# Kernel tuning notes

Hardware: AMD Instinct MI355X
Metric: run time of the kernel (lower is better)

## Reference

```python
import jax, jax.numpy as jnp
import numpy as np

EMB = 1024
HEADS = 16
HEAD_DIM = EMB // HEADS
FF = 4 * EMB
B, S = 4, 2048


def gelu_tanh(x):
    c = jnp.sqrt(jnp.asarray(2.0 / jnp.pi, x.dtype))
    return 0.5 * x * (1.0 + jnp.tanh(c * (x + 0.044715 * x ** 3)))


def layernorm(x, g, b, eps=1e-5):
    mu = jnp.mean(x, axis=-1, keepdims=True)
    var = jnp.var(x, axis=-1, keepdims=True)
    return (x - mu) * jax.lax.rsqrt(var + eps) * g + b


def setup_inputs() -> dict:
    key = jax.random.key(0)
    ks = jax.random.split(key, 12)
    s = 0.02
    return {
        "x": jax.random.normal(ks[0], (B, S, EMB), jnp.float32),
        "Wq": jax.random.normal(ks[1], (EMB, EMB), jnp.float32) * s,
        "bq": jnp.zeros((EMB,), jnp.float32),
        "Wk": jax.random.normal(ks[2], (EMB, EMB), jnp.float32) * s,
        "bk": jnp.zeros((EMB,), jnp.float32),
        "Wv": jax.random.normal(ks[3], (EMB, EMB), jnp.float32) * s,
        "bv": jnp.zeros((EMB,), jnp.float32),
        "Wo": jax.random.normal(ks[4], (EMB, EMB), jnp.float32) * s,
        "bo": jnp.zeros((EMB,), jnp.float32),
        "W1": jax.random.normal(ks[5], (EMB, FF), jnp.float32) * s,
        "b1": jnp.zeros((FF,), jnp.float32),
        "W2": jax.random.normal(ks[6], (FF, EMB), jnp.float32) * s,
        "b2": jnp.zeros((EMB,), jnp.float32),
        "g1": jnp.ones((EMB,), jnp.float32),
        "be1": jnp.zeros((EMB,), jnp.float32),
        "g2": jnp.ones((EMB,), jnp.float32),
        "be2": jnp.zeros((EMB,), jnp.float32),
    }


def reference(x, Wq, bq, Wk, bk, Wv, bv, Wo, bo, W1, b1, W2, b2, g1, be1, g2, be2):
    b, s, _ = x.shape
    shortcut = x
    h = layernorm(x, g1, be1)
    # QKV projections -> [b, heads, s, head_dim]
    def proj(W, bias):
        return (h @ W + bias).reshape(b, s, HEADS, HEAD_DIM).transpose(0, 2, 1, 3)
    q, k, v = proj(Wq, bq), proj(Wk, bk), proj(Wv, bv)
    scores = jnp.einsum('bhqd,bhkd->bhqk', q, k) / jnp.sqrt(jnp.asarray(HEAD_DIM, x.dtype))
    causal = jnp.triu(jnp.ones((s, s), bool), k=1)  # True above diagonal -> masked
    scores = jnp.where(causal, -jnp.inf, scores)
    probs = jax.nn.softmax(scores, axis=-1)  # dropout p=0 -> identity
    ctx = jnp.einsum('bhqk,bhkd->bhqd', probs, v).transpose(0, 2, 1, 3).reshape(b, s, EMB)
    attn_out = ctx @ Wo + bo
    x = attn_out + shortcut
    shortcut = x
    h = layernorm(x, g2, be2)
    ff = gelu_tanh(h @ W1 + b1) @ W2 + b2
    return ff + shortcut
```

## Files before the change

kernel.cpp:

```cpp
#include <hip/hip_runtime.h>
#include <hip/hip_bf16.h>

#define EMB 1024
#define HEADS 16
#define HDIM 64
#define FFDIM 4096
#define BSZ 4
#define SEQ 2048
#define MROWS (BSZ * SEQ)
#define QKVW 3072
#define VSTRIDE 2080

typedef __attribute__((ext_vector_type(8))) short bf16x8;
typedef __attribute__((ext_vector_type(4))) float f32x4;
typedef __attribute__((ext_vector_type(16))) float f32x16;
typedef __attribute__((ext_vector_type(4))) unsigned short u16x4;
typedef unsigned short u16;

__device__ __forceinline__ float bf2f(u16 u) {
  union { unsigned int i; float f; } c; c.i = ((unsigned int)u) << 16; return c.f;
}
__device__ __forceinline__ u16 f2bf(float f) {
  union { float f; unsigned int i; } c; c.f = f;
  unsigned int i = c.i + 0x7fff + ((c.i >> 16) & 1);
  return (u16)(i >> 16);
}
__device__ __forceinline__ unsigned fbits(float f) {
  union { float f; unsigned u; } c; c.f = f; return c.u;
}
__device__ __forceinline__ unsigned pk2(float e0, float e1) {
  return (fbits(e0) >> 16) | (fbits(e1) & 0xffff0000u);
}
__device__ __forceinline__ f32x16 zero16() {
  f32x16 z;
#pragma unroll
  for (int i = 0; i < 16; ++i) z[i] = 0.f;
  return z;
}
__device__ __forceinline__ void gload16(const u16* g, void* lds) {
  __builtin_amdgcn_global_load_lds(
      (const __attribute__((address_space(1))) void*)g,
      (__attribute__((address_space(3))) void*)lds, 16, 0, 0);
}

__global__ __launch_bounds__(256) void ln_kernel(
    const float* __restrict__ x, const float* __restrict__ g,
    const float* __restrict__ be, u16* __restrict__ out) {
  int w = threadIdx.x >> 6, l = threadIdx.x & 63;
  size_t row = (size_t)blockIdx.x * 4 + w;
  const float* xr = x + row * EMB;
  float f[4][4];
  float s = 0.f, s2 = 0.f;
#pragma unroll
  for (int c = 0; c < 4; ++c) {
    f32x4 v = *(const f32x4*)(xr + c * 256 + l * 4);
#pragma unroll
    for (int j = 0; j < 4; ++j) {
      f[c][j] = v[j];
      s += v[j];
      s2 += v[j] * v[j];
    }
  }
#pragma unroll
  for (int m = 1; m < 64; m <<= 1) {
    s  += __shfl_xor(s, m);
    s2 += __shfl_xor(s2, m);
  }
  float mu = s * (1.f / EMB);
  float var = s2 * (1.f / EMB) - mu * mu;
  float rs = rsqrtf(var + 1e-5f);
#pragma unroll
  for (int c = 0; c < 4; ++c) {
    u16x4 o;
#pragma unroll
    for (int j = 0; j < 4; ++j) {
      int col = c * 256 + l * 4 + j;
      o[j] = f2bf((f[c][j] - mu) * rs * g[col] + be[col]);
    }
    *(u16x4*)(out + row * EMB + c * 256 + l * 4) = o;
  }
}

__global__ __launch_bounds__(256) void transpose_cvt(
    const float* __restrict__ in, u16* __restrict__ out, int R, int C) {
  __shared__ u16 tile[32][33];
  int c0 = blockIdx.x * 32, r0 = blockIdx.y * 32;
  int tx = threadIdx.x, ty = threadIdx.y;
#pragma unroll
  for (int i = ty; i < 32; i += 8)
    tile[i][tx] = f2bf(in[(size_t)(r0 + i) * C + c0 + tx]);
  __syncthreads();
#pragma unroll
  for (int i = ty; i < 32; i += 8)
    out[(size_t)(c0 + i) * R + r0 + tx] = tile[tx][i];
}

__global__ __launch_bounds__(256) void concat_bias(
    const float* __restrict__ a, const float* __restrict__ b,
    const float* __restrict__ c, float* __restrict__ o) {
  int i = blockIdx.x * 256 + threadIdx.x;
  o[i] = i < 1024 ? a[i] : (i < 2048 ? b[i - 1024] : c[i - 2048]);
}

__global__ __launch_bounds__(256) void transpose_v(
    const u16* __restrict__ QKV, u16* __restrict__ Vt) {
  __shared__ u16 tile[32][33];
  int s0 = blockIdx.x * 32, d0 = blockIdx.y * 32, bh = blockIdx.z;
  int h = bh % HEADS, b = bh / HEADS;
  int tx = threadIdx.x, ty = threadIdx.y;
  const u16* src = QKV + (size_t)b * SEQ * QKVW + 2048 + h * HDIM;
  u16* dst = Vt + (size_t)bh * HDIM * VSTRIDE;
#pragma unroll
  for (int i = ty; i < 32; i += 8)
    tile[i][tx] = src[(size_t)(s0 + i) * QKVW + d0 + tx];
  __syncthreads();
#pragma unroll
  for (int i = ty; i < 32; i += 8)
    dst[(size_t)(d0 + i) * VSTRIDE + s0 + tx] = tile[tx][i];
}

__device__ __forceinline__ float gelu_f(float v) {
  float u = 1.5957691216057308f * (v + 0.044715f * v * v * v);
  return v / (1.f + __expf(-u));
}

template <int EPI, typename OT>
__global__ __launch_bounds__(256, 3) void gemm32(
    const u16* __restrict__ A, const u16* __restrict__ Bt,
    const float* __restrict__ bias, const float* __restrict__ res,
    OT* __restrict__ C, int N, int K) {
  __shared__ char lds[32768];
  char* ldsA = lds;
  char* ldsB = lds + 16384;
  int nbn = N >> 7;
  int cpx = gridDim.x >> 3;
  int bid = blockIdx.x;
  int logical = (bid & 7) * cpx + (bid >> 3);
  int mb = logical / nbn, nb = logical % nbn;
  int m0 = mb << 7, n0 = nb << 7;
  int t = threadIdx.x, w = t >> 6, l = t & 63;
  int wr = w >> 1, wc = w & 1;
  int l31 = l & 31, lh = l >> 5;
  int srow8 = l >> 3, sp8 = l & 7;

  f32x16 acc[2][2] = {{zero16(), zero16()}, {zero16(), zero16()}};

  for (int k0 = 0; k0 < K; k0 += 64) {
    __syncthreads();
#pragma unroll
    for (int ps = 0; ps < 4; ++ps) {
      int r = ps * 32 + (w << 3) + srow8;
      int sc = (sp8 ^ (r & 7)) << 3;
      gload16(A + (size_t)(m0 + r) * K + k0 + sc, ldsA + ps * 4096 + (w << 10));
      gload16(Bt + (size_t)(n0 + r) * K + k0 + sc, ldsB + ps * 4096 + (w << 10));
    }
    __syncthreads();
#pragma unroll
    for (int hf = 0; hf < 2; ++hf) {
      bf16x8 afr[2][2], bfr[2][2];
#pragma unroll
      for (int blk = 0; blk < 2; ++blk)
#pragma unroll
        for (int kk = 0; kk < 2; ++kk) {
          int kki = hf * 2 + kk;
          int ra = (wr << 6) + (blk << 5) + l31;
          int rb = (wc << 6) + (blk << 5) + l31;
          int pa = (((kki << 1) + lh) ^ (ra & 7)) << 4;
          int pb = (((kki << 1) + lh) ^ (rb & 7)) << 4;
          afr[blk][kk] = *(const bf16x8*)(ldsA + ra * 128 + pa);
          bfr[blk][kk] = *(const bf16x8*)(ldsB + rb * 128 + pb);
        }
#pragma unroll
      for (int m = 0; m < 2; ++m)
#pragma unroll
        for (int n = 0; n < 2; ++n)
#pragma unroll
          for (int kk = 0; kk < 2; ++kk)
            acc[m][n] = __builtin_amdgcn_mfma_f32_32x32x16_bf16(
                afr[m][kk], bfr[n][kk], acc[m][n], 0, 0, 0);
    }
  }

#pragma unroll
  for (int m = 0; m < 2; ++m)
#pragma unroll
    for (int n = 0; n < 2; ++n) {
      int col = n0 + (wc << 6) + (n << 5) + l31;
      float bcol = bias[col];
      int rbase = m0 + (wr << 6) + (m << 5) + (lh << 2);
#pragma unroll
      for (int reg = 0; reg < 16; ++reg) {
        int row = rbase + (reg & 3) + ((reg >> 2) << 3);
        float v = acc[m][n][reg] + bcol;
        if (EPI & 2) v = gelu_f(v);
        if (EPI & 1) v += res[(size_t)row * N + col];
        if (sizeof(OT) == 2)
          C[(size_t)row * N + col] = (OT)f2bf(v);
        else
          C[(size_t)row * N + col] = (OT)v;
      }
    }
}

#define QKT(ACCS, QF)                                                       \
  do {                                                                      \
    ACCS = zero16();                                                        \
    __builtin_amdgcn_s_setprio(1);                                          \
    _Pragma("unroll") for (int s_ = 0; s_ < 4; ++s_)                        \
        ACCS = __builtin_amdgcn_mfma_f32_32x32x16_bf16(kf[s_], QF[s_],      \
                                                       ACCS, 0, 0, 0);      \
    __builtin_amdgcn_s_setprio(0);                                          \
  } while (0)

#define STEP(ACCS, L, O0, O1, DIAG)                                         \
  do {                                                                      \
    float e_[16];                                                           \
    _Pragma("unroll") for (int i = 0; i < 16; ++i) {                        \
      float sv = ACCS[i];                                                   \
      if (DIAG) {                                                           \
        int kvl = (i & 3) + 8 * (i >> 2) + 4 * g;                           \
        if (kvl > lq) sv = -1e30f;                                          \
      }                                                                     \
      e_[i] = __expf(sv);                                                   \
    }                                                                       \
    float ts = 0.f;                                                         \
    _Pragma("unroll") for (int i = 0; i < 16; ++i) ts += e_[i];             \
    ts += __shfl_xor(ts, 32);                                               \
    L += ts;                                                                \
    _Pragma("unroll") for (int s_ = 0; s_ < 2; ++s_) {                      \
      unsigned plo0 = pk2(e_[8 * s_ + 0], e_[8 * s_ + 1]);                  \
      unsigned plo1 = pk2(e_[8 * s_ + 2], e_[8 * s_ + 3]);                  \
      unsigned phi0 = pk2(e_[8 * s_ + 4], e_[8 * s_ + 5]);                  \
      unsigned phi1 = pk2(e_[8 * s_ + 6], e_[8 * s_ + 7]);                  \
      unsigned recv0 = __shfl_xor(g ? plo0 : phi0, 32);                     \
      unsigned recv1 = __shfl_xor(g ? plo1 : phi1, 32);                     \
      union { unsigned u[4]; bf16x8 v; } pf_;                               \
      pf_.u[0] = g ? recv0 : plo0;                                          \
      pf_.u[1] = g ? recv1 : plo1;                                          \
      pf_.u[2] = g ? phi0 : recv0;                                          \
      pf_.u[3] = g ? phi1 : recv1;                                          \
      __builtin_amdgcn_s_setprio(1);                                        \
      O0 = __builtin_amdgcn_mfma_f32_32x32x16_bf16(vf0[s_], pf_.v, O0,      \
                                                   0, 0, 0);                \
      O1 = __builtin_amdgcn_mfma_f32_32x32x16_bf16(vf1[s_], pf_.v, O1,      \
                                                   0, 0, 0);                \
      __builtin_amdgcn_s_setprio(0);                                        \
    }                                                                       \
  } while (0)

#define STAGE(KV0, BUF)                                                     \
  do {                                                                      \
    char* sb_ = myslab + (BUF) * 8192;                                      \
    _Pragma("unroll") for (int i_ = 0; i_ < 4; ++i_) {                      \
      int r_ = i_ * 8 + (l >> 3);                                           \
      gload16(Kp + (size_t)((KV0) + r_) * QKVW + (((l & 7) ^ (r_ & 7)) << 3),\
              sb_ + i_ * 1024);                                             \
    }                                                                       \
    _Pragma("unroll") for (int i_ = 0; i_ < 4; ++i_) {                      \
      int r_ = i_ * 16 + (l >> 2);                                          \
      gload16(Vt + (size_t)r_ * VSTRIDE + (KV0) + (((l & 3) ^ (r_ & 3)) << 3),\
              sb_ + 4096 + i_ * 1024);                                      \
    }                                                                       \
  } while (0)

#define RDFRAGS(BUF)                                                        \
  do {                                                                      \
    const char* sb_ = myslab + (BUF) * 8192;                                \
    _Pragma("unroll") for (int s_ = 0; s_ < 4; ++s_) {                      \
      int c_ = s_ * 2 + g;                                                  \
      kf[s_] = *(const bf16x8*)(sb_ + lq * 128 + ((c_ ^ (lq & 7)) << 4));   \
    }                                                                       \
    _Pragma("unroll") for (int s_ = 0; s_ < 2; ++s_) {                      \
      int c_ = s_ * 2 + g;                                                  \
      vf0[s_] = *(const bf16x8*)(sb_ + 4096 + lq * 64 +                     \
                                 ((c_ ^ (lq & 3)) << 4));                   \
      vf1[s_] = *(const bf16x8*)(sb_ + 4096 + (32 + lq) * 64 +              \
                                 ((c_ ^ (lq & 3)) << 4));                   \
    }                                                                       \
  } while (0)

#define WRITE_OUT(O0, O1, L, WQ0)                                           \
  do {                                                                      \
    float inv = 1.f / L;                                                    \
    u16* orow = Op + (size_t)((WQ0) + lq) * EMB;                            \
    _Pragma("unroll") for (int dblk = 0; dblk < 2; ++dblk) {                \
      _Pragma("unroll") for (int p = 0; p < 8; ++p) {                       \
        int i0 = 2 * p;                                                     \
        int d = dblk * 32 + 2 * (p & 1) + 8 * (p >> 1) + 4 * g;             \
        float v0 = (dblk ? O1[i0] : O0[i0]) * inv;                          \
        float v1 = (dblk ? O1[i0 + 1] : O0[i0 + 1]) * inv;                  \
        unsigned wd = (unsigned)f2bf(v0) | ((unsigned)f2bf(v1) << 16);      \
        *(unsigned*)(orow + d) = wd;                                        \
      }                                                                     \
    }                                                                       \
  } while (0)

__global__ __launch_bounds__(256, 2) void attn_kernel(
    const u16* __restrict__ QKV, const u16* __restrict__ VtG,
    u16* __restrict__ O) {
  __shared__ char slabs[4][16384];
  int t = threadIdx.x, w = t >> 6, l = t & 63;
  int lq = l & 31, g = l >> 5;
  char* myslab = slabs[w];
  int wid = blockIdx.x * 4 + w;
  int qi = wid & 31, bh = wid >> 5;
  int h = bh & (HEADS - 1), b = bh >> 4;
  int wq0a = qi * 32, wq0b = (63 - qi) * 32;
  int ntA = qi + 1, ntB = 64 - qi;
  const u16* Qp = QKV + (size_t)b * SEQ * QKVW + h * HDIM;
  const u16* Kp = QKV + (size_t)b * SEQ * QKVW + 1024 + h * HDIM;
  const u16* Vt = VtG + (size_t)bh * HDIM * VSTRIDE;
  u16* Op = O + (size_t)b * SEQ * EMB + h * HDIM;

  bf16x8 qfA[4], qfB[4];
#pragma unroll
  for (int s = 0; s < 4; ++s) {
    bf16x8 ra = *(const bf16x8*)(Qp + (size_t)(wq0a + lq) * QKVW + s * 16 + g * 8);
    bf16x8 rb = *(const bf16x8*)(Qp + (size_t)(wq0b + lq) * QKVW + s * 16 + g * 8);
#pragma unroll
    for (int j = 0; j < 8; ++j) {
      qfA[s][j] = (short)f2bf(bf2f((u16)ra[j]) * 0.125f);
      qfB[s][j] = (short)f2bf(bf2f((u16)rb[j]) * 0.125f);
    }
  }

  f32x16 oA0 = zero16(), oA1 = zero16(), oB0 = zero16(), oB1 = zero16();
  f32x16 sA, sB;
  float lA = 0.f, lB = 0.f;
  bf16x8 kf[4], vf0[2], vf1[2];

  STAGE(0, 0);
  for (int ti = 0; ti < ntA; ++ti) {
    STAGE((ti + 1) * 32, (ti + 1) & 1);
    asm volatile("s_waitcnt vmcnt(8)" ::: "memory");
    RDFRAGS(ti & 1);
    QKT(sA, qfA);
    QKT(sB, qfB);
    bool diagA = (ti == ntA - 1);
    STEP(sA, lA, oA0, oA1, diagA);
    STEP(sB, lB, oB0, oB1, false);
  }
  WRITE_OUT(oA0, oA1, lA, wq0a);
  for (int ti = ntA; ti < ntB; ++ti) {
    if (ti + 1 < ntB) {
      STAGE((ti + 1) * 32, (ti + 1) & 1);
      asm volatile("s_waitcnt vmcnt(8)" ::: "memory");
    } else {
      asm volatile("s_waitcnt vmcnt(0)" ::: "memory");
    }
    RDFRAGS(ti & 1);
    QKT(sB, qfB);
    bool diagB = (ti == ntB - 1);
    STEP(sB, lB, oB0, oB1, diagB);
  }
  WRITE_OUT(oB0, oB1, lB, wq0b);
}

extern "C" void kernel_launch(void* const* d_in, const int* in_sizes, int n_in,
                              void* d_out, int out_size, void* d_ws, size_t ws_size,
                              hipStream_t stream) {
  (void)in_sizes; (void)n_in; (void)out_size; (void)ws_size;
  const float* x   = (const float*)d_in[0];
  const float* Wq  = (const float*)d_in[1];
  const float* bq  = (const float*)d_in[2];
  const float* Wk  = (const float*)d_in[3];
  const float* bk  = (const float*)d_in[4];
  const float* Wv  = (const float*)d_in[5];
  const float* bv  = (const float*)d_in[6];
  const float* Wo  = (const float*)d_in[7];
  const float* bo  = (const float*)d_in[8];
  const float* W1  = (const float*)d_in[9];
  const float* b1  = (const float*)d_in[10];
  const float* W2  = (const float*)d_in[11];
  const float* b2  = (const float*)d_in[12];
  const float* g1  = (const float*)d_in[13];
  const float* be1 = (const float*)d_in[14];
  const float* g2  = (const float*)d_in[15];
  const float* be2 = (const float*)d_in[16];

  char* ws = (char*)d_ws;
  const size_t MB = 1ull << 20;
  u16*   WqkvT = (u16*)(ws + 0 * MB);
  u16*   WoT   = (u16*)(ws + 6 * MB);
  u16*   W1T   = (u16*)(ws + 8 * MB);
  u16*   W2T   = (u16*)(ws + 16 * MB);
  float* bqkv  = (float*)(ws + 24 * MB);
  u16*   hbuf  = (u16*)(ws + 25 * MB);
  float* x1f   = (float*)(ws + 41 * MB);
  u16*   qkv   = (u16*)(ws + 73 * MB);
  u16*   VtG   = (u16*)(ws + 121 * MB);
  u16*   gbuf  = (u16*)(ws + 73 * MB);

  dim3 tb(32, 8);
  transpose_cvt<<<dim3(EMB / 32, EMB / 32), tb, 0, stream>>>(Wq, WqkvT, EMB, EMB);
  transpose_cvt<<<dim3(EMB / 32, EMB / 32), tb, 0, stream>>>(Wk, WqkvT + 1024 * 1024, EMB, EMB);
  transpose_cvt<<<dim3(EMB / 32, EMB / 32), tb, 0, stream>>>(Wv, WqkvT + 2 * 1024 * 1024, EMB, EMB);
  transpose_cvt<<<dim3(EMB / 32, EMB / 32), tb, 0, stream>>>(Wo, WoT, EMB, EMB);
  transpose_cvt<<<dim3(FFDIM / 32, EMB / 32), tb, 0, stream>>>(W1, W1T, EMB, FFDIM);
  transpose_cvt<<<dim3(EMB / 32, FFDIM / 32), tb, 0, stream>>>(W2, W2T, FFDIM, EMB);
  concat_bias<<<12, 256, 0, stream>>>(bq, bk, bv, bqkv);

  ln_kernel<<<MROWS / 4, 256, 0, stream>>>(x, g1, be1, hbuf);

  gemm32<0, u16><<<(MROWS / 128) * (QKVW / 128), 256, 0, stream>>>(
      hbuf, WqkvT, bqkv, nullptr, qkv, QKVW, EMB);

  transpose_v<<<dim3(SEQ / 32, HDIM / 32, BSZ * HEADS), tb, 0, stream>>>(qkv, VtG);

  attn_kernel<<<BSZ * HEADS * (SEQ / 64) / 4, 256, 0, stream>>>(qkv, VtG, hbuf);

  gemm32<1, float><<<(MROWS / 128) * (EMB / 128), 256, 0, stream>>>(
      hbuf, WoT, bo, x, x1f, EMB, EMB);

  ln_kernel<<<MROWS / 4, 256, 0, stream>>>(x1f, g2, be2, hbuf);

  gemm32<2, u16><<<(MROWS / 128) * (FFDIM / 128), 256, 0, stream>>>(
      hbuf, W1T, b1, nullptr, gbuf, FFDIM, EMB);
  gemm32<1, float><<<(MROWS / 128) * (EMB / 128), 256, 0, stream>>>(
      gbuf, W2T, b2, x1f, (float*)d_out, EMB, FFDIM);
}
```

Before: 409.5 us.

## Use 2-wave GEMM blocks with 64x128 per-wave tiles

```diff
diff --git a/kernel.cpp b/kernel.cpp
--- a/kernel.cpp
+++ b/kernel.cpp
@@ -125,13 +125,11 @@
 }
 
 template <int EPI, typename OT>
-__global__ __launch_bounds__(256, 3) void gemm32(
+__global__ __launch_bounds__(128) void gemm32(
     const u16* __restrict__ A, const u16* __restrict__ Bt,
     const float* __restrict__ bias, const float* __restrict__ res,
     OT* __restrict__ C, int N, int K) {
   __shared__ char lds[32768];
-  char* ldsA = lds;
-  char* ldsB = lds + 16384;
   int nbn = N >> 7;
   int cpx = gridDim.x >> 3;
   int bid = blockIdx.x;
@@ -139,59 +137,66 @@
   int mb = logical / nbn, nb = logical % nbn;
   int m0 = mb << 7, n0 = nb << 7;
   int t = threadIdx.x, w = t >> 6, l = t & 63;
-  int wr = w >> 1, wc = w & 1;
   int l31 = l & 31, lh = l >> 5;
-  int srow8 = l >> 3, sp8 = l & 7;
-
-  f32x16 acc[2][2] = {{zero16(), zero16()}, {zero16(), zero16()}};
+  int srow8 = t >> 3, sp8 = t & 7;
+
+  f32x16 acc[2][4];
+#pragma unroll
+  for (int i = 0; i < 2; ++i)
+#pragma unroll
+    for (int j = 0; j < 4; ++j) acc[i][j] = zero16();
 
   for (int k0 = 0; k0 < K; k0 += 64) {
     __syncthreads();
 #pragma unroll
-    for (int ps = 0; ps < 4; ++ps) {
-      int r = ps * 32 + (w << 3) + srow8;
+    for (int i = 0; i < 8; ++i) {
+      int r = i * 16 + srow8;
       int sc = (sp8 ^ (r & 7)) << 3;
-      gload16(A + (size_t)(m0 + r) * K + k0 + sc, ldsA + ps * 4096 + (w << 10));
-      gload16(Bt + (size_t)(n0 + r) * K + k0 + sc, ldsB + ps * 4096 + (w << 10));
+      gload16(A + (size_t)(m0 + r) * K + k0 + sc, lds + i * 2048 + (w << 10));
+      gload16(Bt + (size_t)(n0 + r) * K + k0 + sc,
+              lds + 16384 + i * 2048 + (w << 10));
     }
     __syncthreads();
 #pragma unroll
     for (int hf = 0; hf < 2; ++hf) {
-      bf16x8 afr[2][2], bfr[2][2];
+      bf16x8 afr[2][2], bfr[4][2];
+#pragma unroll
+      for (int kk = 0; kk < 2; ++kk) {
+        int c = ((hf * 2 + kk) << 1) + lh;
+#pragma unroll
+        for (int blk = 0; blk < 2; ++blk) {
+          int ra = (w << 6) + (blk << 5) + l31;
+          afr[blk][kk] = *(const bf16x8*)(lds + ra * 128 + ((c ^ (ra & 7)) << 4));
+        }
+#pragma unroll
+        for (int n = 0; n < 4; ++n) {
+          int rb = (n << 5) + l31;
+          bfr[n][kk] = *(const bf16x8*)(lds + 16384 + rb * 128 +
+                                        ((c ^ (rb & 7)) << 4));
+        }
+      }
 #pragma unroll
       for (int blk = 0; blk < 2; ++blk)
 #pragma unroll
-        for (int kk = 0; kk < 2; ++kk) {
-          int kki = hf * 2 + kk;
-          int ra = (wr << 6) + (blk << 5) + l31;
-          int rb = (wc << 6) + (blk << 5) + l31;
-          int pa = (((kki << 1) + lh) ^ (ra & 7)) << 4;
-          int pb = (((kki << 1) + lh) ^ (rb & 7)) << 4;
-          afr[blk][kk] = *(const bf16x8*)(ldsA + ra * 128 + pa);
-          bfr[blk][kk] = *(const bf16x8*)(ldsB + rb * 128 + pb);
-        }
-#pragma unroll
-      for (int m = 0; m < 2; ++m)
-#pragma unroll
-        for (int n = 0; n < 2; ++n)
+        for (int n = 0; n < 4; ++n)
 #pragma unroll
           for (int kk = 0; kk < 2; ++kk)
-            acc[m][n] = __builtin_amdgcn_mfma_f32_32x32x16_bf16(
-                afr[m][kk], bfr[n][kk], acc[m][n], 0, 0, 0);
-    }
-  }
-
-#pragma unroll
-  for (int m = 0; m < 2; ++m)
-#pragma unroll
-    for (int n = 0; n < 2; ++n) {
-      int col = n0 + (wc << 6) + (n << 5) + l31;
+            acc[blk][n] = __builtin_amdgcn_mfma_f32_32x32x16_bf16(
+                afr[blk][kk], bfr[n][kk], acc[blk][n], 0, 0, 0);
+    }
+  }
+
+#pragma unroll
+  for (int blk = 0; blk < 2; ++blk)
+#pragma unroll
+    for (int n = 0; n < 4; ++n) {
+      int col = n0 + (n << 5) + l31;
       float bcol = bias[col];
-      int rbase = m0 + (wr << 6) + (m << 5) + (lh << 2);
+      int rbase = m0 + (w << 6) + (blk << 5) + (lh << 2);
 #pragma unroll
       for (int reg = 0; reg < 16; ++reg) {
         int row = rbase + (reg & 3) + ((reg >> 2) << 3);
-        float v = acc[m][n][reg] + bcol;
+        float v = acc[blk][n][reg] + bcol;
         if (EPI & 2) v = gelu_f(v);
         if (EPI & 1) v += res[(size_t)row * N + col];
         if (sizeof(OT) == 2)
@@ -402,20 +407,20 @@
 
   ln_kernel<<<MROWS / 4, 256, 0, stream>>>(x, g1, be1, hbuf);
 
-  gemm32<0, u16><<<(MROWS / 128) * (QKVW / 128), 256, 0, stream>>>(
+  gemm32<0, u16><<<(MROWS / 128) * (QKVW / 128), 128, 0, stream>>>(
       hbuf, WqkvT, bqkv, nullptr, qkv, QKVW, EMB);
 
   transpose_v<<<dim3(SEQ / 32, HDIM / 32, BSZ * HEADS), tb, 0, stream>>>(qkv, VtG);
 
   attn_kernel<<<BSZ * HEADS * (SEQ / 64) / 4, 256, 0, stream>>>(qkv, VtG, hbuf);
 
-  gemm32<1, float><<<(MROWS / 128) * (EMB / 128), 256, 0, stream>>>(
+  gemm32<1, float><<<(MROWS / 128) * (EMB / 128), 128, 0, stream>>>(
       hbuf, WoT, bo, x, x1f, EMB, EMB);
 
   ln_kernel<<<MROWS / 4, 256, 0, stream>>>(x1f, g2, be2, hbuf);
 
-  gemm32<2, u16><<<(MROWS / 128) * (FFDIM / 128), 256, 0, stream>>>(
+  gemm32<2, u16><<<(MROWS / 128) * (FFDIM / 128), 128, 0, stream>>>(
       hbuf, W1T, b1, nullptr, gbuf, FFDIM, EMB);
-  gemm32<1, float><<<(MROWS / 128) * (EMB / 128), 256, 0, stream>>>(
+  gemm32<1, float><<<(MROWS / 128) * (EMB / 128), 128, 0, stream>>>(
       gbuf, W2T, b2, x1f, (float*)d_out, EMB, FFDIM);
 }
```

Result: slower. 451.2 us (+10.2%).
